# Optimization experiments

Hardware: AMD Instinct MI355X
Metric: run time of the kernel (lower is better)

The kernel has to match this reference:

```python
import jax, jax.numpy as jnp
import numpy as np

DIM = 1024
NUM_EXPERTS = 8
TOP_K = 2
HIDDEN = DIM * 2
B, S = 2, 4096


def setup_inputs() -> dict:
    key = jax.random.key(0)
    ks = jax.random.split(key, 8)
    sd = 1.0 / np.sqrt(DIM)
    sh = 1.0 / np.sqrt(HIDDEN)
    return {
        "x": jax.random.normal(ks[0], (B, S, DIM), dtype=jnp.float32),
        "gate_w": jax.random.uniform(ks[1], (NUM_EXPERTS, DIM), jnp.float32, -sd, sd),
        "gate_b": jax.random.uniform(ks[2], (NUM_EXPERTS,), jnp.float32, -sd, sd),
        "W1": jax.random.uniform(ks[3], (NUM_EXPERTS, DIM, HIDDEN), jnp.float32, -sd, sd),
        "b1": jax.random.uniform(ks[4], (NUM_EXPERTS, HIDDEN), jnp.float32, -sd, sd),
        "W2": jax.random.uniform(ks[5], (NUM_EXPERTS, HIDDEN, DIM), jnp.float32, -sh, sh),
        "b2": jax.random.uniform(ks[6], (NUM_EXPERTS, DIM), jnp.float32, -sh, sh),
    }


def reference(x, gate_w, gate_b, W1, b1, W2, b2):
    Bd, Sd, D = x.shape
    xf = x.reshape(-1, D)                                  # [T, D]
    T = xf.shape[0]
    logits = xf @ gate_w.T + gate_b                        # [T, E]
    weights = jax.nn.softmax(logits.astype(jnp.float32), axis=-1)
    topk_w, topk_i = jax.lax.top_k(weights, TOP_K)         # [T, K]
    topk_w = topk_w / topk_w.sum(axis=-1, keepdims=True)
    # combine weights scattered back to dense [T, E] (top-k indices are distinct)
    comb = jnp.zeros((T, NUM_EXPERTS), topk_w.dtype)
    comb = comb.at[jnp.arange(T)[:, None], topk_i].add(topk_w)
    # dense all-expert FFN (exact GELU, matching nn.GELU default)
    h = jax.nn.gelu(jnp.einsum('td,edh->eth', xf, W1) + b1[:, None, :], approximate=False)
    y = jnp.einsum('eth,ehd->etd', h, W2) + b2[:, None, :]  # [E, T, D]
    out = jnp.einsum('etd,te->td', y, comb.astype(y.dtype)).reshape(Bd, Sd, D)
    return out, logits
```

## Files before the change

kernel.cpp:

```cpp
#include <hip/hip_runtime.h>
#include <math.h>

#define T_TOK 8192
#define DIMX 1024
#define NE 8
#define HID 2048
#define NPAIR (T_TOK * 2)
#define P_PAD (NPAIR + NE * 128)
#define GATE_TPB 32

typedef __attribute__((ext_vector_type(8))) short s16x8;
typedef __attribute__((ext_vector_type(4))) float f32x4;

static __device__ __forceinline__ unsigned short f2bf(float f) {
    union { float f; unsigned u; } v; v.f = f;
    unsigned r = v.u + 0x7FFFu + ((v.u >> 16) & 1u);
    return (unsigned short)(r >> 16);
}
static __device__ __forceinline__ float bf2f(unsigned short u) {
    union { unsigned u; float f; } v; v.u = (unsigned)u << 16; return v.f;
}

static __device__ __forceinline__ float gelu_fast(float v) {
    float u2 = -1.5957691216057308f * v * (1.f + 0.044715f * v * v);
    return v * __builtin_amdgcn_rcpf(1.f + __expf(u2));
}

static __device__ __forceinline__ void gload16(const unsigned short* g, unsigned short* l) {
    __builtin_amdgcn_global_load_lds(
        (const __attribute__((address_space(1))) unsigned int*)g,
        (__attribute__((address_space(3))) unsigned int*)l, 16, 0, 0);
}

__global__ void init_routing_kernel(int* slot_token, float* slot_weight, int* counts) {
    int i = blockIdx.x * blockDim.x + threadIdx.x;
    if (i < P_PAD) { slot_token[i] = 0; slot_weight[i] = 0.f; }
    if (i < NE) counts[i] = 0;
}

__global__ __launch_bounds__(256) void conv_transpose_kernel(
    const float* __restrict__ src, unsigned short* __restrict__ dst, int R, int C) {
    __shared__ float tile[64][65];
    int e = blockIdx.z;
    int r0 = blockIdx.y * 64, c0 = blockIdx.x * 64;
    const float* s = src + (size_t)e * R * C;
    unsigned short* d = dst + (size_t)e * R * C;
    int tid = threadIdx.x;
    int lr = tid >> 4, lc4 = (tid & 15) * 4;
    #pragma unroll
    for (int it = 0; it < 4; it++) {
        float4 v = *(const float4*)&s[(size_t)(r0 + it * 16 + lr) * C + c0 + lc4];
        tile[it * 16 + lr][lc4 + 0] = v.x;
        tile[it * 16 + lr][lc4 + 1] = v.y;
        tile[it * 16 + lr][lc4 + 2] = v.z;
        tile[it * 16 + lr][lc4 + 3] = v.w;
    }
    __syncthreads();
    int cc = tid >> 3, rch = (tid & 7) * 8;
    #pragma unroll
    for (int it = 0; it < 2; it++) {
        int c = it * 32 + cc;
        unsigned short r[8];
        #pragma unroll
        for (int j = 0; j < 8; j++) r[j] = f2bf(tile[rch + j][c]);
        *(uint4*)&d[(size_t)(c0 + c) * R + r0 + rch] = *(const uint4*)&r[0];
    }
}

__global__ __launch_bounds__(256) void gate_kernel(
    const float* __restrict__ x, const float* __restrict__ gw, const float* __restrict__ gb,
    float* __restrict__ logits_out, int* counts, int* __restrict__ pair_epos,
    float* __restrict__ pair_w, unsigned short* __restrict__ xb) {
    __shared__ float sgw[NE * DIMX];
    __shared__ int lcount[NE], lbase[NE];
    __shared__ int s_e[GATE_TPB * 2];
    __shared__ int s_lp[GATE_TPB * 2];
    __shared__ float s_wv[GATE_TPB * 2];
    int tid = threadIdx.x;
    for (int i = tid; i < NE * DIMX / 4; i += 256)
        ((float4*)sgw)[i] = ((const float4*)gw)[i];
    if (tid < NE) lcount[tid] = 0;
    __syncthreads();

    int wave = tid >> 6, lane = tid & 63;
    int tbase = blockIdx.x * GATE_TPB;
    for (int r = 0; r < GATE_TPB / 4; ++r) {
        int ti = wave * (GATE_TPB / 4) + r;
        int t = tbase + ti;
        const float* xr = x + (size_t)t * DIMX;
        float acc[NE] = {};
        #pragma unroll
        for (int i = 0; i < DIMX / 256; i++) {
            float4 xv = *(const float4*)&xr[i * 256 + lane * 4];
            unsigned short rb[4] = { f2bf(xv.x), f2bf(xv.y), f2bf(xv.z), f2bf(xv.w) };
            *(uint2*)&xb[(size_t)t * DIMX + i * 256 + lane * 4] = *(const uint2*)&rb[0];
            #pragma unroll
            for (int e = 0; e < NE; e++) {
                float4 wv = *(const float4*)&sgw[e * DIMX + i * 256 + lane * 4];
                acc[e] += xv.x * wv.x + xv.y * wv.y + xv.z * wv.z + xv.w * wv.w;
            }
        }
        #pragma unroll
        for (int e = 0; e < NE; e++) {
            #pragma unroll
            for (int off = 32; off; off >>= 1) acc[e] += __shfl_xor(acc[e], off);
        }
        if (lane == 0) {
            float* lo = logits_out + (size_t)t * NE;
            #pragma unroll
            for (int e = 0; e < NE; e++) { acc[e] += gb[e]; lo[e] = acc[e]; }
            float l0 = acc[0]; int e0 = 0;
            #pragma unroll
            for (int e = 1; e < NE; e++) if (acc[e] > l0) { l0 = acc[e]; e0 = e; }
            float l1 = -1e30f; int e1 = -1;
            #pragma unroll
            for (int e = 0; e < NE; e++) if (e != e0 && acc[e] > l1) { l1 = acc[e]; e1 = e; }
            float q = expf(l1 - l0);
            float wn0 = 1.f / (1.f + q);
            float wn1 = q / (1.f + q);
            int lp0 = atomicAdd(&lcount[e0], 1);
            int lp1 = atomicAdd(&lcount[e1], 1);
            s_e[ti * 2] = e0; s_lp[ti * 2] = lp0; s_wv[ti * 2] = wn0;
            s_e[ti * 2 + 1] = e1; s_lp[ti * 2 + 1] = lp1; s_wv[ti * 2 + 1] = wn1;
        }
    }
    __syncthreads();
    if (tid < NE) lbase[tid] = atomicAdd(&counts[tid], lcount[tid]);
    __syncthreads();
    if (tid < GATE_TPB * 2) {
        int e = s_e[tid];
        int gp = lbase[e] + s_lp[tid];
        int gi = (tbase + (tid >> 1)) * 2 + (tid & 1);
        pair_epos[gi] = (e << 28) | gp;
        pair_w[gi] = s_wv[tid];
    }
}

__global__ void scan_kernel(const int* counts, int* offsets) {
    if (threadIdx.x == 0 && blockIdx.x == 0) {
        int o = 0;
        offsets[0] = 0;
        for (int e = 0; e < NE; e++) { o += (counts[e] + 127) & ~127; offsets[e + 1] = o; }
    }
}

__global__ void place_kernel(const int* __restrict__ pair_epos, const float* __restrict__ pair_w,
                             const int* __restrict__ offsets, int* __restrict__ slot_token,
                             float* __restrict__ slot_weight, int* __restrict__ tok2slot) {
    int p = blockIdx.x * 256 + threadIdx.x;
    if (p >= NPAIR) return;
    int ep = pair_epos[p];
    int e = ep >> 28;
    int pos = ep & 0x0FFFFFFF;
    int slot = offsets[e] + pos;
    slot_token[slot] = p >> 1;
    slot_weight[slot] = pair_w[p];
    tok2slot[p] = slot;
}

#define BARRIER() asm volatile("s_barrier" ::: "memory")
#define WAIT_VM(n) asm volatile("s_waitcnt vmcnt(" #n ")" ::: "memory")
#define WAIT_LGKM0() do { asm volatile("s_waitcnt lgkmcnt(0)" ::: "memory"); \
                          __builtin_amdgcn_sched_barrier(0); } while (0)


__global__ __launch_bounds__(512, 4) void gemm1_kernel(
    const unsigned short* __restrict__ xb, const unsigned short* __restrict__ W1t,
    const float* __restrict__ b1, const int* __restrict__ offsets,
    const int* __restrict__ slot_token, unsigned short* __restrict__ hbuf) {
    int e = blockIdx.x;
    int row_base = offsets[e];
    int rows = offsets[e + 1] - row_base;
    int m0 = blockIdx.z * 128;
    if (m0 >= rows) return;
    int n0 = blockIdx.y * 128;

    __shared__ unsigned short sA[2][128 * 32];
    __shared__ unsigned short sB[2][128 * 32];

    int tid = threadIdx.x;
    const unsigned short* w1e = W1t + (size_t)e * HID * DIMX;

    int srow = tid >> 2;
    int kperm = (tid & 3) ^ ((tid >> 3) & 3);
    int tok = slot_token[row_base + m0 + srow];
    const unsigned short* gA0 = xb + (size_t)tok * DIMX + kperm * 8;
    const unsigned short* gB0 = w1e + (size_t)(n0 + srow) * DIMX + kperm * 8;

#define STG1(b, k0) do { \
        gload16(gA0 + (k0), &sA[b][tid * 8]); \
        gload16(gB0 + (k0), &sB[b][tid * 8]); \
    } while (0)

    f32x4 acc[4][2] = {};
    int wid = tid >> 6; int wr = wid >> 2, wc = wid & 3;
    int lane = tid & 63; int lr = lane & 15, lg = lane >> 4;
    int kx8 = (lg ^ ((lr >> 1) & 3)) * 8;

#define CMP1(CUR) do { \
        s16x8 af[4], bfr[2]; \
        _Pragma("unroll") \
        for (int m = 0; m < 4; m++) af[m] = *(const s16x8*)&sA[CUR][(wr * 64 + m * 16 + lr) * 32 + kx8]; \
        _Pragma("unroll") \
        for (int n = 0; n < 2; n++) bfr[n] = *(const s16x8*)&sB[CUR][(wc * 32 + n * 16 + lr) * 32 + kx8]; \
        __builtin_amdgcn_s_setprio(1); \
        _Pragma("unroll") \
        for (int m = 0; m < 4; m++) { \
            _Pragma("unroll") \
            for (int n = 0; n < 2; n++) \
                acc[m][n] = __builtin_amdgcn_mfma_f32_16x16x32_bf16(af[m], bfr[n], acc[m][n], 0, 0, 0); \
        } \
        __builtin_amdgcn_s_setprio(0); \
    } while (0)

    const int NT = DIMX / 32;
    STG1(0, 0);
    int cur = 0;
    for (int t = 0; t < NT - 1; ++t) {
        STG1(cur ^ 1, (t + 1) * 32);
        WAIT_VM(2);
        BARRIER();
        CMP1(cur);
        WAIT_LGKM0();
        BARRIER();
        cur ^= 1;
    }
    WAIT_VM(0);
    BARRIER();
    CMP1(cur);
#undef STG1
#undef CMP1

    #pragma unroll
    for (int m = 0; m < 4; m++) {
        #pragma unroll
        for (int n = 0; n < 2; n++) {
            int col = n0 + wc * 32 + n * 16 + lr;
            float bias = b1[e * HID + col];
            #pragma unroll
            for (int i = 0; i < 4; i++) {
                int row = wr * 64 + m * 16 + lg * 4 + i;
                float v = gelu_fast(acc[m][n][i] + bias);
                hbuf[(size_t)(row_base + m0 + row) * HID + col] = f2bf(v);
            }
        }
    }
}

__global__ __launch_bounds__(512, 4) void gemm2_kernel(
    const unsigned short* __restrict__ hbuf, const unsigned short* __restrict__ W2t,
    const float* __restrict__ b2, const int* __restrict__ offsets,
    const float* __restrict__ slot_weight, unsigned short* __restrict__ ybuf) {
    int e = blockIdx.x;
    int row_base = offsets[e];
    int rows = offsets[e + 1] - row_base;
    int m0 = blockIdx.z * 128;
    if (m0 >= rows) return;
    int n0 = blockIdx.y * 128;

    __shared__ unsigned short sA[2][128 * 32];
    __shared__ unsigned short sB[2][128 * 32];
    __shared__ float s_w[128];

    int tid = threadIdx.x;
    if (tid < 128) s_w[tid] = slot_weight[row_base + m0 + tid];

    const unsigned short* ha = hbuf + (size_t)(row_base + m0) * HID;
    const unsigned short* w2e = W2t + (size_t)e * DIMX * HID;

    int srow = tid >> 2;
    int kperm = (tid & 3) ^ ((tid >> 3) & 3);
    const unsigned short* gA0 = ha + (size_t)srow * HID + kperm * 8;
    const unsigned short* gB0 = w2e + (size_t)(n0 + srow) * HID + kperm * 8;

#define STG2(b, k0) do { \
        gload16(gA0 + (k0), &sA[b][tid * 8]); \
        gload16(gB0 + (k0), &sB[b][tid * 8]); \
    } while (0)

    f32x4 acc[4][2] = {};
    int wid = tid >> 6; int wr = wid >> 2, wc = wid & 3;
    int lane = tid & 63; int lr = lane & 15, lg = lane >> 4;
    int kx8 = (lg ^ ((lr >> 1) & 3)) * 8;

#define CMP2(CUR) do { \
        s16x8 af[4], bfr[2]; \
        _Pragma("unroll") \
        for (int m = 0; m < 4; m++) af[m] = *(const s16x8*)&sA[CUR][(wr * 64 + m * 16 + lr) * 32 + kx8]; \
        _Pragma("unroll") \
        for (int n = 0; n < 2; n++) bfr[n] = *(const s16x8*)&sB[CUR][(wc * 32 + n * 16 + lr) * 32 + kx8]; \
        __builtin_amdgcn_s_setprio(1); \
        _Pragma("unroll") \
        for (int m = 0; m < 4; m++) { \
            _Pragma("unroll") \
            for (int n = 0; n < 2; n++) \
                acc[m][n] = __builtin_amdgcn_mfma_f32_16x16x32_bf16(af[m], bfr[n], acc[m][n], 0, 0, 0); \
        } \
        __builtin_amdgcn_s_setprio(0); \
    } while (0)

    const int NT = HID / 32;
    STG2(0, 0);
    int cur = 0;
    for (int t = 0; t < NT - 1; ++t) {
        STG2(cur ^ 1, (t + 1) * 32);
        WAIT_VM(2);
        BARRIER();
        CMP2(cur);
        WAIT_LGKM0();
        BARRIER();
        cur ^= 1;
    }
    WAIT_VM(0);
    BARRIER();
    CMP2(cur);
#undef STG2
#undef CMP2

    #pragma unroll
    for (int m = 0; m < 4; m++) {
        #pragma unroll
        for (int n = 0; n < 2; n++) {
            int col = n0 + wc * 32 + n * 16 + lr;
            float bias = b2[e * DIMX + col];
            #pragma unroll
            for (int i = 0; i < 4; i++) {
                int row = wr * 64 + m * 16 + lg * 4 + i;
                float v = (acc[m][n][i] + bias) * s_w[row];
                ybuf[(size_t)(row_base + m0 + row) * DIMX + col] = f2bf(v);
            }
        }
    }
}

__global__ __launch_bounds__(256) void combine_kernel(
    const unsigned short* __restrict__ ybuf, const int* __restrict__ tok2slot,
    float* __restrict__ out) {
    int t = blockIdx.x;
    int d = threadIdx.x * 4;
    int sa = tok2slot[t * 2], sb = tok2slot[t * 2 + 1];
    ushort4 a = *(const ushort4*)&ybuf[(size_t)sa * DIMX + d];
    ushort4 b = *(const ushort4*)&ybuf[(size_t)sb * DIMX + d];
    float4 o;
    o.x = bf2f(a.x) + bf2f(b.x);
    o.y = bf2f(a.y) + bf2f(b.y);
    o.z = bf2f(a.z) + bf2f(b.z);
    o.w = bf2f(a.w) + bf2f(b.w);
    *(float4*)&out[(size_t)t * DIMX + d] = o;
}

extern "C" void kernel_launch(void* const* d_in, const int* in_sizes, int n_in,
                              void* d_out, int out_size, void* d_ws, size_t ws_size,
                              hipStream_t stream) {
    const float* x  = (const float*)d_in[0];
    const float* gw = (const float*)d_in[1];
    const float* gb = (const float*)d_in[2];
    const float* W1 = (const float*)d_in[3];
    const float* b1 = (const float*)d_in[4];
    const float* W2 = (const float*)d_in[5];
    const float* b2 = (const float*)d_in[6];
    float* out = (float*)d_out;
    float* logits = out + (size_t)T_TOK * DIMX;

    char* ws = (char*)d_ws;
    unsigned short* W2t = (unsigned short*)ws; ws += (size_t)NE * DIMX * HID * 2;
    unsigned short* W1t = (unsigned short*)ws;
    unsigned short* ybuf = (unsigned short*)ws; ws += (size_t)NE * DIMX * HID * 2;
    unsigned short* xb = (unsigned short*)ws; ws += (size_t)T_TOK * DIMX * 2;
    unsigned short* hbuf = (unsigned short*)ws; ws += (size_t)P_PAD * HID * 2;
    int* counts = (int*)ws; ws += 256;
    int* offsets = (int*)ws; ws += 256;
    int* pair_epos = (int*)ws; ws += (size_t)NPAIR * 4;
    float* pair_w = (float*)ws; ws += (size_t)NPAIR * 4;
    int* slot_token = (int*)ws; ws += (size_t)P_PAD * 4;
    float* slot_weight = (float*)ws; ws += (size_t)P_PAD * 4;
    int* tok2slot = (int*)ws; ws += (size_t)NPAIR * 4;

    init_routing_kernel<<<(P_PAD + 255) / 256, 256, 0, stream>>>(slot_token, slot_weight, counts);
    conv_transpose_kernel<<<dim3(HID / 64, DIMX / 64, NE), 256, 0, stream>>>(W1, W1t, DIMX, HID);
    conv_transpose_kernel<<<dim3(DIMX / 64, HID / 64, NE), 256, 0, stream>>>(W2, W2t, HID, DIMX);
    gate_kernel<<<T_TOK / GATE_TPB, 256, 0, stream>>>(x, gw, gb, logits, counts, pair_epos,
                                                      pair_w, xb);
    scan_kernel<<<1, 1, 0, stream>>>(counts, offsets);
    place_kernel<<<NPAIR / 256, 256, 0, stream>>>(pair_epos, pair_w, offsets, slot_token,
                                                  slot_weight, tok2slot);
    gemm1_kernel<<<dim3(NE, HID / 128, 128), 512, 0, stream>>>(xb, W1t, b1, offsets, slot_token, hbuf);
    gemm2_kernel<<<dim3(NE, DIMX / 128, 128), 512, 0, stream>>>(hbuf, W2t, b2, offsets, slot_weight, ybuf);
    combine_kernel<<<T_TOK, 256, 0, stream>>>(ybuf, tok2slot, out);
}
```

Before: 276.1 us.

## Enlarge MoE GEMM tiles to 256x256x64 with phased LDS-staged pipeline

Both expert GEMMs move from 128x128 tiles with K-step 32 to 256x256 tiles with K-step 64. Each wave now accumulates an 8x4 grid of MFMA fragments, and the K-loop is split into four phases that overlap half-tile prefetches with compute. Expert padding grows to 256 rows to match, and the grid z-dimension is cut to 33. The goal is more data reuse per global and LDS load and fewer barriers per FLOP, at the cost of 128KB of LDS per block, lower occupancy (launch bounds 2) and more padded rows of wasted work.

```diff
diff --git a/kernel.cpp b/kernel.cpp
--- a/kernel.cpp
+++ b/kernel.cpp
@@ -6,7 +6,7 @@
 #define NE 8
 #define HID 2048
 #define NPAIR (T_TOK * 2)
-#define P_PAD (NPAIR + NE * 128)
+#define P_PAD (NPAIR + NE * 256)
 #define GATE_TPB 32
 
 typedef __attribute__((ext_vector_type(8))) short s16x8;
@@ -140,7 +140,7 @@
     if (threadIdx.x == 0 && blockIdx.x == 0) {
         int o = 0;
         offsets[0] = 0;
-        for (int e = 0; e < NE; e++) { o += (counts[e] + 127) & ~127; offsets[e + 1] = o; }
+        for (int e = 0; e < NE; e++) { o += (counts[e] + 255) & ~255; offsets[e + 1] = o; }
     }
 }
 
@@ -163,170 +163,202 @@
 #define WAIT_LGKM0() do { asm volatile("s_waitcnt lgkmcnt(0)" ::: "memory"); \
                           __builtin_amdgcn_sched_barrier(0); } while (0)
 
-
-__global__ __launch_bounds__(512, 4) void gemm1_kernel(
+#define PH(CUR, KXO, MH, DOB, ...) do { \
+    if (DOB) { \
+        _Pragma("unroll") \
+        for (int n = 0; n < 4; n++) \
+            b_[n] = *(const s16x8*)&sB[CUR][(wc * 64 + n * 16 + lr) * 64 + (KXO)]; \
+    } \
+    _Pragma("unroll") \
+    for (int m = 0; m < 4; m++) \
+        a_[m] = *(const s16x8*)&sA[CUR][(wr * 128 + (MH) * 64 + m * 16 + lr) * 64 + (KXO)]; \
+    __VA_ARGS__; \
+    BARRIER(); \
+    WAIT_LGKM0(); \
+    __builtin_amdgcn_s_setprio(1); \
+    _Pragma("unroll") \
+    for (int m = 0; m < 4; m++) { \
+        _Pragma("unroll") \
+        for (int n = 0; n < 4; n++) \
+            acc[(MH) * 4 + m][n] = __builtin_amdgcn_mfma_f32_16x16x32_bf16(a_[m], b_[n], acc[(MH) * 4 + m][n], 0, 0, 0); \
+    } \
+    __builtin_amdgcn_s_setprio(0); \
+} while (0)
+
+__global__ __launch_bounds__(512, 2) void gemm1_kernel(
     const unsigned short* __restrict__ xb, const unsigned short* __restrict__ W1t,
     const float* __restrict__ b1, const int* __restrict__ offsets,
     const int* __restrict__ slot_token, unsigned short* __restrict__ hbuf) {
     int e = blockIdx.x;
     int row_base = offsets[e];
     int rows = offsets[e + 1] - row_base;
-    int m0 = blockIdx.z * 128;
+    int m0 = blockIdx.z * 256;
     if (m0 >= rows) return;
-    int n0 = blockIdx.y * 128;
-
-    __shared__ unsigned short sA[2][128 * 32];
-    __shared__ unsigned short sB[2][128 * 32];
+    int n0 = blockIdx.y * 256;
+
+    __shared__ unsigned short sA[2][256 * 64];
+    __shared__ unsigned short sB[2][256 * 64];
 
     int tid = threadIdx.x;
     const unsigned short* w1e = W1t + (size_t)e * HID * DIMX;
 
-    int srow = tid >> 2;
-    int kperm = (tid & 3) ^ ((tid >> 3) & 3);
-    int tok = slot_token[row_base + m0 + srow];
-    const unsigned short* gA0 = xb + (size_t)tok * DIMX + kperm * 8;
-    const unsigned short* gB0 = w1e + (size_t)(n0 + srow) * DIMX + kperm * 8;
-
-#define STG1(b, k0) do { \
+    int r0 = tid >> 3;
+    int kp = (tid & 7) ^ (r0 & 7);
+    int tok0 = slot_token[row_base + m0 + r0];
+    int tok1 = slot_token[row_base + m0 + r0 + 64];
+    int tok2 = slot_token[row_base + m0 + r0 + 128];
+    int tok3 = slot_token[row_base + m0 + r0 + 192];
+    const unsigned short* gA0 = xb + (size_t)tok0 * DIMX + kp * 8;
+    const unsigned short* gA1 = xb + (size_t)tok1 * DIMX + kp * 8;
+    const unsigned short* gA2 = xb + (size_t)tok2 * DIMX + kp * 8;
+    const unsigned short* gA3 = xb + (size_t)tok3 * DIMX + kp * 8;
+    const unsigned short* gB0 = w1e + (size_t)(n0 + r0) * DIMX + kp * 8;
+    const unsigned short* gB1 = w1e + (size_t)(n0 + r0 + 64) * DIMX + kp * 8;
+    const unsigned short* gB2 = w1e + (size_t)(n0 + r0 + 128) * DIMX + kp * 8;
+    const unsigned short* gB3 = w1e + (size_t)(n0 + r0 + 192) * DIMX + kp * 8;
+
+#define STG4a(b, k0) do { \
         gload16(gA0 + (k0), &sA[b][tid * 8]); \
+        gload16(gA1 + (k0), &sA[b][tid * 8 + 4096]); \
         gload16(gB0 + (k0), &sB[b][tid * 8]); \
+        gload16(gB1 + (k0), &sB[b][tid * 8 + 4096]); \
     } while (0)
-
-    f32x4 acc[4][2] = {};
+#define STG4b(b, k0) do { \
+        gload16(gA2 + (k0), &sA[b][tid * 8 + 8192]); \
+        gload16(gA3 + (k0), &sA[b][tid * 8 + 12288]); \
+        gload16(gB2 + (k0), &sB[b][tid * 8 + 8192]); \
+        gload16(gB3 + (k0), &sB[b][tid * 8 + 12288]); \
+    } while (0)
+
+    f32x4 acc[8][4] = {};
     int wid = tid >> 6; int wr = wid >> 2, wc = wid & 3;
     int lane = tid & 63; int lr = lane & 15, lg = lane >> 4;
-    int kx8 = (lg ^ ((lr >> 1) & 3)) * 8;
-
-#define CMP1(CUR) do { \
-        s16x8 af[4], bfr[2]; \
-        _Pragma("unroll") \
-        for (int m = 0; m < 4; m++) af[m] = *(const s16x8*)&sA[CUR][(wr * 64 + m * 16 + lr) * 32 + kx8]; \
-        _Pragma("unroll") \
-        for (int n = 0; n < 2; n++) bfr[n] = *(const s16x8*)&sB[CUR][(wc * 32 + n * 16 + lr) * 32 + kx8]; \
-        __builtin_amdgcn_s_setprio(1); \
-        _Pragma("unroll") \
-        for (int m = 0; m < 4; m++) { \
-            _Pragma("unroll") \
-            for (int n = 0; n < 2; n++) \
-                acc[m][n] = __builtin_amdgcn_mfma_f32_16x16x32_bf16(af[m], bfr[n], acc[m][n], 0, 0, 0); \
-        } \
-        __builtin_amdgcn_s_setprio(0); \
-    } while (0)
-
-    const int NT = DIMX / 32;
-    STG1(0, 0);
-    int cur = 0;
-    for (int t = 0; t < NT - 1; ++t) {
-        STG1(cur ^ 1, (t + 1) * 32);
-        WAIT_VM(2);
-        BARRIER();
-        CMP1(cur);
-        WAIT_LGKM0();
-        BARRIER();
-        cur ^= 1;
-    }
+    int kx0 = (lg ^ (lr & 7)) * 8;
+    s16x8 b_[4], a_[4];
+
+    const int NT = DIMX / 64;
+    STG4a(0, 0); STG4b(0, 0);
     WAIT_VM(0);
     BARRIER();
-    CMP1(cur);
-#undef STG1
-#undef CMP1
+    int cur = 0;
+    for (int t = 0; t < NT; ++t) {
+        int nxt = cur ^ 1;
+        int k0n = (t + 1) * 64;
+        bool pf = (t + 1 < NT);
+        PH(cur, kx0, 0, 1, if (pf) STG4a(nxt, k0n));
+        BARRIER();
+        PH(cur, kx0, 1, 0, (void)0);
+        BARRIER();
+        PH(cur, kx0 ^ 32, 0, 1, if (pf) STG4b(nxt, k0n));
+        BARRIER();
+        PH(cur, kx0 ^ 32, 1, 0, (void)0);
+        WAIT_VM(0);
+        BARRIER();
+        cur = nxt;
+    }
+#undef STG4a
+#undef STG4b
 
     #pragma unroll
-    for (int m = 0; m < 4; m++) {
+    for (int n = 0; n < 4; n++) {
+        int col = n0 + wc * 64 + n * 16 + lr;
+        float bias = b1[e * HID + col];
         #pragma unroll
-        for (int n = 0; n < 2; n++) {
-            int col = n0 + wc * 32 + n * 16 + lr;
-            float bias = b1[e * HID + col];
+        for (int M = 0; M < 8; M++) {
             #pragma unroll
             for (int i = 0; i < 4; i++) {
-                int row = wr * 64 + m * 16 + lg * 4 + i;
-                float v = gelu_fast(acc[m][n][i] + bias);
+                int row = wr * 128 + M * 16 + lg * 4 + i;
+                float v = gelu_fast(acc[M][n][i] + bias);
                 hbuf[(size_t)(row_base + m0 + row) * HID + col] = f2bf(v);
             }
         }
     }
 }
 
-__global__ __launch_bounds__(512, 4) void gemm2_kernel(
+__global__ __launch_bounds__(512, 2) void gemm2_kernel(
     const unsigned short* __restrict__ hbuf, const unsigned short* __restrict__ W2t,
     const float* __restrict__ b2, const int* __restrict__ offsets,
     const float* __restrict__ slot_weight, unsigned short* __restrict__ ybuf) {
     int e = blockIdx.x;
     int row_base = offsets[e];
     int rows = offsets[e + 1] - row_base;
-    int m0 = blockIdx.z * 128;
+    int m0 = blockIdx.z * 256;
     if (m0 >= rows) return;
-    int n0 = blockIdx.y * 128;
-
-    __shared__ unsigned short sA[2][128 * 32];
-    __shared__ unsigned short sB[2][128 * 32];
-    __shared__ float s_w[128];
+    int n0 = blockIdx.y * 256;
+
+    __shared__ unsigned short sA[2][256 * 64];
+    __shared__ unsigned short sB[2][256 * 64];
+    __shared__ float s_w[256];
 
     int tid = threadIdx.x;
-    if (tid < 128) s_w[tid] = slot_weight[row_base + m0 + tid];
+    if (tid < 256) s_w[tid] = slot_weight[row_base + m0 + tid];
 
     const unsigned short* ha = hbuf + (size_t)(row_base + m0) * HID;
     const unsigned short* w2e = W2t + (size_t)e * DIMX * HID;
 
-    int srow = tid >> 2;
-    int kperm = (tid & 3) ^ ((tid >> 3) & 3);
-    const unsigned short* gA0 = ha + (size_t)srow * HID + kperm * 8;
-    const unsigned short* gB0 = w2e + (size_t)(n0 + srow) * HID + kperm * 8;
-
-#define STG2(b, k0) do { \
+    int r0 = tid >> 3;
+    int kp = (tid & 7) ^ (r0 & 7);
+    const unsigned short* gA0 = ha + (size_t)r0 * HID + kp * 8;
+    const unsigned short* gA1 = ha + (size_t)(r0 + 64) * HID + kp * 8;
+    const unsigned short* gA2 = ha + (size_t)(r0 + 128) * HID + kp * 8;
+    const unsigned short* gA3 = ha + (size_t)(r0 + 192) * HID + kp * 8;
+    const unsigned short* gB0 = w2e + (size_t)(n0 + r0) * HID + kp * 8;
+    const unsigned short* gB1 = w2e + (size_t)(n0 + r0 + 64) * HID + kp * 8;
+    const unsigned short* gB2 = w2e + (size_t)(n0 + r0 + 128) * HID + kp * 8;
+    const unsigned short* gB3 = w2e + (size_t)(n0 + r0 + 192) * HID + kp * 8;
+
+#define STG4a(b, k0) do { \
         gload16(gA0 + (k0), &sA[b][tid * 8]); \
+        gload16(gA1 + (k0), &sA[b][tid * 8 + 4096]); \
         gload16(gB0 + (k0), &sB[b][tid * 8]); \
+        gload16(gB1 + (k0), &sB[b][tid * 8 + 4096]); \
     } while (0)
-
-    f32x4 acc[4][2] = {};
+#define STG4b(b, k0) do { \
+        gload16(gA2 + (k0), &sA[b][tid * 8 + 8192]); \
+        gload16(gA3 + (k0), &sA[b][tid * 8 + 12288]); \
+        gload16(gB2 + (k0), &sB[b][tid * 8 + 8192]); \
+        gload16(gB3 + (k0), &sB[b][tid * 8 + 12288]); \
+    } while (0)
+
+    f32x4 acc[8][4] = {};
     int wid = tid >> 6; int wr = wid >> 2, wc = wid & 3;
     int lane = tid & 63; int lr = lane & 15, lg = lane >> 4;
-    int kx8 = (lg ^ ((lr >> 1) & 3)) * 8;
-
-#define CMP2(CUR) do { \
-        s16x8 af[4], bfr[2]; \
-        _Pragma("unroll") \
-        for (int m = 0; m < 4; m++) af[m] = *(const s16x8*)&sA[CUR][(wr * 64 + m * 16 + lr) * 32 + kx8]; \
-        _Pragma("unroll") \
-        for (int n = 0; n < 2; n++) bfr[n] = *(const s16x8*)&sB[CUR][(wc * 32 + n * 16 + lr) * 32 + kx8]; \
-        __builtin_amdgcn_s_setprio(1); \
-        _Pragma("unroll") \
-        for (int m = 0; m < 4; m++) { \
-            _Pragma("unroll") \
-            for (int n = 0; n < 2; n++) \
-                acc[m][n] = __builtin_amdgcn_mfma_f32_16x16x32_bf16(af[m], bfr[n], acc[m][n], 0, 0, 0); \
-        } \
-        __builtin_amdgcn_s_setprio(0); \
-    } while (0)
-
-    const int NT = HID / 32;
-    STG2(0, 0);
-    int cur = 0;
-    for (int t = 0; t < NT - 1; ++t) {
-        STG2(cur ^ 1, (t + 1) * 32);
-        WAIT_VM(2);
-        BARRIER();
-        CMP2(cur);
-        WAIT_LGKM0();
-        BARRIER();
-        cur ^= 1;
-    }
+    int kx0 = (lg ^ (lr & 7)) * 8;
+    s16x8 b_[4], a_[4];
+
+    const int NT = HID / 64;
+    STG4a(0, 0); STG4b(0, 0);
     WAIT_VM(0);
     BARRIER();
-    CMP2(cur);
-#undef STG2
-#undef CMP2
+    int cur = 0;
+    for (int t = 0; t < NT; ++t) {
+        int nxt = cur ^ 1;
+        int k0n = (t + 1) * 64;
+        bool pf = (t + 1 < NT);
+        PH(cur, kx0, 0, 1, if (pf) STG4a(nxt, k0n));
+        BARRIER();
+        PH(cur, kx0, 1, 0, (void)0);
+        BARRIER();
+        PH(cur, kx0 ^ 32, 0, 1, if (pf) STG4b(nxt, k0n));
+        BARRIER();
+        PH(cur, kx0 ^ 32, 1, 0, (void)0);
+        WAIT_VM(0);
+        BARRIER();
+        cur = nxt;
+    }
+#undef STG4a
+#undef STG4b
 
     #pragma unroll
-    for (int m = 0; m < 4; m++) {
+    for (int n = 0; n < 4; n++) {
+        int col = n0 + wc * 64 + n * 16 + lr;
+        float bias = b2[e * DIMX + col];
         #pragma unroll
-        for (int n = 0; n < 2; n++) {
-            int col = n0 + wc * 32 + n * 16 + lr;
-            float bias = b2[e * DIMX + col];
+        for (int M = 0; M < 8; M++) {
             #pragma unroll
             for (int i = 0; i < 4; i++) {
-                int row = wr * 64 + m * 16 + lg * 4 + i;
-                float v = (acc[m][n][i] + bias) * s_w[row];
+                int row = wr * 128 + M * 16 + lg * 4 + i;
+                float v = (acc[M][n][i] + bias) * s_w[row];
                 ybuf[(size_t)(row_base + m0 + row) * DIMX + col] = f2bf(v);
             }
         }
@@ -384,7 +416,7 @@
     scan_kernel<<<1, 1, 0, stream>>>(counts, offsets);
     place_kernel<<<NPAIR / 256, 256, 0, stream>>>(pair_epos, pair_w, offsets, slot_token,
                                                   slot_weight, tok2slot);
-    gemm1_kernel<<<dim3(NE, HID / 128, 128), 512, 0, stream>>>(xb, W1t, b1, offsets, slot_token, hbuf);
-    gemm2_kernel<<<dim3(NE, DIMX / 128, 128), 512, 0, stream>>>(hbuf, W2t, b2, offsets, slot_weight, ybuf);
+    gemm1_kernel<<<dim3(NE, HID / 256, 33), 512, 0, stream>>>(xb, W1t, b1, offsets, slot_token, hbuf);
+    gemm2_kernel<<<dim3(NE, DIMX / 256, 33), 512, 0, stream>>>(hbuf, W2t, b2, offsets, slot_weight, ybuf);
     combine_kernel<<<T_TOK, 256, 0, stream>>>(ybuf, tok2slot, out);
 }
```

New measurement: 326.1 us. 18.1% more time.
